# Performance work log

Hardware: AMD Instinct MI355X
Metric: run time of the kernel (lower is better)

## Reference

```python
import jax, jax.numpy as jnp
import numpy as np

NUM_FEATURES = 2048
NUM_SAMPLES = 16384
SOURCE_CLASSES = 1024
TEMP = 0.05
MOMENTUM = 0.2
BATCH = 256
SPECIAL_LABEL = 5554  # hard-coded remap in the original forward (is_source=True path)


def setup_inputs() -> dict:
    key = jax.random.key(0)
    k1, k2, k3 = jax.random.split(key, 3)
    inputs = jax.random.normal(k1, (BATCH, NUM_FEATURES), dtype=jnp.float32)
    inputs = inputs / jnp.linalg.norm(inputs, axis=1, keepdims=True)  # re-ID features are L2-normalized
    targets = jax.random.randint(k2, (BATCH,), 0, NUM_SAMPLES)  # 1-based labels; 0 -> invalid after -1 shift
    features = jax.random.normal(k3, (NUM_SAMPLES, NUM_FEATURES), dtype=jnp.float32)
    features = features / jnp.linalg.norm(features, axis=1, keepdims=True)
    return {"inputs": inputs, "targets": targets, "features": features}


def reference(inputs, targets, features):
    ignore = SOURCE_CLASSES - 1
    t = targets - 1
    t = jnp.where(t == SPECIAL_LABEL, ignore, t)  # remap special label to ignore_index class
    # torch drops rows with t < 0 before the mm and cross_entropy ignores ignore_index;
    # rows are independent under row-wise softmax, so masking is equivalent to filtering.
    valid = (t >= 0) & (t != ignore)
    logits = (inputs @ features.T) / TEMP  # [B, NUM_SAMPLES]
    logp = jax.nn.log_softmax(logits, axis=-1)
    tc = jnp.clip(t, 0, NUM_SAMPLES - 1)
    nll = -jnp.take_along_axis(logp, tc[:, None], axis=1)[:, 0]  # [B]
    n_valid = jnp.sum(valid)
    loss = jnp.sum(jnp.where(valid, nll, 0.0)) / jnp.maximum(n_valid, 1).astype(nll.dtype)
    return loss
```

## Files before the change

### kernel.cpp

```cpp
#include <hip/hip_runtime.h>
#include <hip/hip_bf16.h>

typedef __attribute__((ext_vector_type(4))) float f32x4;
typedef __attribute__((ext_vector_type(8))) short s16x8;

#define M_DIM 256
#define N_DIM 16384
#define K_DIM 2048
#define BM 128
#define BN 128
#define BK 32
#define LDS_PITCH 40
#define NKT (K_DIM / BK)
#define TEMP_INV 20.0f
#define SPECIAL 5554
#define IGNORE_IDX 1023

__device__ __forceinline__ short f2bf(float x) {
  __hip_bfloat16 h = __float2bfloat16(x);
  return __builtin_bit_cast(short, h);
}

__device__ __forceinline__ void cvt_store(short* dst, const float4& f0, const float4& f1) {
  s16x8 h;
  h[0] = f2bf(f0.x); h[1] = f2bf(f0.y); h[2] = f2bf(f0.z); h[3] = f2bf(f0.w);
  h[4] = f2bf(f1.x); h[5] = f2bf(f1.y); h[6] = f2bf(f1.z); h[7] = f2bf(f1.w);
  *reinterpret_cast<s16x8*>(dst) = h;
}

__global__ __launch_bounds__(512, 1) void gemm_logits(
    const float* __restrict__ A, const float* __restrict__ B,
    float* __restrict__ C) {
  __shared__ __align__(16) short As[2][BM * LDS_PITCH];
  __shared__ __align__(16) short Bs[2][BN * LDS_PITCH];

  int bid = blockIdx.x;
  int lbid = (bid & 7) * 32 + (bid >> 3);
  int bm = lbid & 1;
  int bn = lbid >> 1;

  int tid = threadIdx.x;
  int wave = tid >> 6;
  int lane = tid & 63;
  int wm = wave >> 2;
  int wn = wave & 3;

  int srow = tid >> 2;
  int squad = tid & 3;
  const float* aG = A + (size_t)(bm * BM + srow) * K_DIM + squad * 8;
  const float* bG = B + (size_t)(bn * BN + srow) * K_DIM + squad * 8;
  int swoff = srow * LDS_PITCH + squad * 8;

  f32x4 acc[4][2];
#pragma unroll
  for (int mi = 0; mi < 4; ++mi)
#pragma unroll
    for (int ni = 0; ni < 2; ++ni)
      acc[mi][ni] = f32x4{0.f, 0.f, 0.f, 0.f};

  float4 rA[2][2], rB[2][2];

  rA[0][0] = *(const float4*)(aG);      rA[0][1] = *(const float4*)(aG + 4);
  rB[0][0] = *(const float4*)(bG);      rB[0][1] = *(const float4*)(bG + 4);
  cvt_store(&As[0][swoff], rA[0][0], rA[0][1]);
  cvt_store(&Bs[0][swoff], rB[0][0], rB[0][1]);
  rA[1][0] = *(const float4*)(aG + BK); rA[1][1] = *(const float4*)(aG + BK + 4);
  rB[1][0] = *(const float4*)(bG + BK); rB[1][1] = *(const float4*)(bG + BK + 4);
  __syncthreads();

  int arow0 = (wm * 64 + (lane & 15)) * LDS_PITCH + (lane >> 4) * 8;
  int brow0 = (wn * 32 + (lane & 15)) * LDS_PITCH + (lane >> 4) * 8;

  for (int ktb = 0; ktb < NKT; ktb += 2) {
#pragma unroll
    for (int u = 0; u < 2; ++u) {
      int kt = ktb + u;
      const short* asb = &As[u][0];
      const short* bsb = &Bs[u][0];
      s16x8 af[4], bfr[2];
#pragma unroll
      for (int mi = 0; mi < 4; ++mi)
        af[mi] = *reinterpret_cast<const s16x8*>(asb + arow0 + mi * 16 * LDS_PITCH);
#pragma unroll
      for (int ni = 0; ni < 2; ++ni)
        bfr[ni] = *reinterpret_cast<const s16x8*>(bsb + brow0 + ni * 16 * LDS_PITCH);
#pragma unroll
      for (int mi = 0; mi < 4; ++mi)
#pragma unroll
        for (int ni = 0; ni < 2; ++ni)
          acc[mi][ni] = __builtin_amdgcn_mfma_f32_16x16x32_bf16(
              af[mi], bfr[ni], acc[mi][ni], 0, 0, 0);

      if (kt + 1 < NKT) {
        cvt_store(&As[u ^ 1][swoff], rA[u ^ 1][0], rA[u ^ 1][1]);
        cvt_store(&Bs[u ^ 1][swoff], rB[u ^ 1][0], rB[u ^ 1][1]);
        if (kt + 2 < NKT) {
          const float* ap = aG + (size_t)(kt + 2) * BK;
          const float* bp = bG + (size_t)(kt + 2) * BK;
          rA[u][0] = *(const float4*)ap;  rA[u][1] = *(const float4*)(ap + 4);
          rB[u][0] = *(const float4*)bp;  rB[u][1] = *(const float4*)(bp + 4);
        }
        __syncthreads();
      }
    }
  }

  int gm_base = bm * BM + wm * 64 + ((lane >> 4) << 2);
  int gn_base = bn * BN + wn * 32 + (lane & 15);
#pragma unroll
  for (int mi = 0; mi < 4; ++mi)
#pragma unroll
    for (int ni = 0; ni < 2; ++ni)
#pragma unroll
      for (int r = 0; r < 4; ++r)
        C[(size_t)(gm_base + mi * 16 + r) * N_DIM + gn_base + ni * 16] =
            acc[mi][ni][r] * TEMP_INV;
}

__global__ __launch_bounds__(256) void lse_nll(
    const float* __restrict__ logits, const int* __restrict__ targets,
    float* __restrict__ nll, float* __restrict__ vld) {
  int b = blockIdx.x;
  const float* row = logits + (size_t)b * N_DIM;
  const float4* r4 = reinterpret_cast<const float4*>(row);
  __shared__ float sm[8];
  int tid = threadIdx.x;
  int wid = tid >> 6, lane = tid & 63;

  float mx = -1e30f;
  for (int j = tid; j < N_DIM / 4; j += 256) {
    float4 v = r4[j];
    mx = fmaxf(mx, fmaxf(fmaxf(v.x, v.y), fmaxf(v.z, v.w)));
  }
#pragma unroll
  for (int m = 1; m < 64; m <<= 1) mx = fmaxf(mx, __shfl_xor(mx, m, 64));
  if (lane == 0) sm[wid] = mx;
  __syncthreads();
  if (tid == 0) {
    float m2 = fmaxf(fmaxf(sm[0], sm[1]), fmaxf(sm[2], sm[3]));
    sm[0] = m2;
  }
  __syncthreads();
  mx = sm[0];

  float s = 0.f;
  for (int j = tid; j < N_DIM / 4; j += 256) {
    float4 v = r4[j];
    s += __expf(v.x - mx) + __expf(v.y - mx) + __expf(v.z - mx) + __expf(v.w - mx);
  }
#pragma unroll
  for (int m = 1; m < 64; m <<= 1) s += __shfl_xor(s, m, 64);
  __syncthreads();
  if (lane == 0) sm[wid] = s;
  __syncthreads();
  if (tid == 0) {
    float ss = sm[0] + sm[1] + sm[2] + sm[3];
    int t = targets[b] - 1;
    if (t == SPECIAL) t = IGNORE_IDX;
    bool valid = (t >= 0) && (t != IGNORE_IDX);
    int tc = t < 0 ? 0 : (t > N_DIM - 1 ? N_DIM - 1 : t);
    float lse = mx + __logf(ss);
    float nl = lse - row[tc];
    nll[b] = valid ? nl : 0.0f;
    vld[b] = valid ? 1.0f : 0.0f;
  }
}

__global__ __launch_bounds__(256) void final_reduce(
    const float* __restrict__ nll, const float* __restrict__ vld,
    float* __restrict__ out) {
  int tid = threadIdx.x;
  float s = nll[tid];
  float c = vld[tid];
#pragma unroll
  for (int m = 1; m < 64; m <<= 1) {
    s += __shfl_xor(s, m, 64);
    c += __shfl_xor(c, m, 64);
  }
  __shared__ float ss[4], cc[4];
  int wid = tid >> 6, lane = tid & 63;
  if (lane == 0) { ss[wid] = s; cc[wid] = c; }
  __syncthreads();
  if (tid == 0) {
    float S = ss[0] + ss[1] + ss[2] + ss[3];
    float C = cc[0] + cc[1] + cc[2] + cc[3];
    out[0] = S / fmaxf(C, 1.0f);
  }
}

extern "C" void kernel_launch(void* const* d_in, const int* in_sizes, int n_in,
                              void* d_out, int out_size, void* d_ws, size_t ws_size,
                              hipStream_t stream) {
  const float* inputs   = (const float*)d_in[0];
  const int*   targets  = (const int*)d_in[1];
  const float* features = (const float*)d_in[2];
  float* out = (float*)d_out;

  float* logits = (float*)d_ws;
  float* nll    = logits + (size_t)M_DIM * N_DIM;
  float* vld    = nll + M_DIM;

  gemm_logits<<<dim3(256), dim3(512), 0, stream>>>(inputs, features, logits);
  lse_nll<<<dim3(M_DIM), dim3(256), 0, stream>>>(logits, targets, nll, vld);
  final_reduce<<<dim3(1), dim3(256), 0, stream>>>(nll, vld, out);
}
```

Baseline: 47.35 us.

## Fuse log-sum-exp into GEMM epilogue and drop logits materialization

The GEMM epilogue now computes exp of each scaled logit, reduces per-row partial sums across lanes and waves, and writes one partial per row per column tile. It also captures the target logit directly, so the 16 MB logits matrix is never written or reread and the separate lse kernel is removed. The max subtraction is dropped because normalized inputs and temperature 0.05 bound logits to about ±20, which fits in float exp. That relies on the inputs being L2-normalized, and the finalize kernel now sums 128 partials per row serially.

```diff
diff --git a/kernel.cpp b/kernel.cpp
--- a/kernel.cpp
+++ b/kernel.cpp
@@ -28,11 +28,15 @@
   *reinterpret_cast<s16x8*>(dst) = h;
 }
 
-__global__ __launch_bounds__(512, 1) void gemm_logits(
+__global__ __launch_bounds__(512, 1) void gemm_fused(
     const float* __restrict__ A, const float* __restrict__ B,
-    float* __restrict__ C) {
+    const int* __restrict__ targets,
+    float* __restrict__ partial,
+    float* __restrict__ targ) {
   __shared__ __align__(16) short As[2][BM * LDS_PITCH];
   __shared__ __align__(16) short Bs[2][BN * LDS_PITCH];
+  __shared__ int tcs[BM];
+  __shared__ float rsum[BM][4];
 
   int bid = blockIdx.x;
   int lbid = (bid & 7) * 32 + (bid >> 3);
@@ -44,6 +48,13 @@
   int lane = tid & 63;
   int wm = wave >> 2;
   int wn = wave & 3;
+
+  if (tid < BM) {
+    int tt = targets[bm * BM + tid] - 1;
+    if (tt == SPECIAL) tt = IGNORE_IDX;
+    int tc = tt < 0 ? 0 : (tt > N_DIM - 1 ? N_DIM - 1 : tt);
+    tcs[tid] = tc;
+  }
 
   int srow = tid >> 2;
   int squad = tid & 3;
@@ -105,83 +116,56 @@
     }
   }
 
-  int gm_base = bm * BM + wm * 64 + ((lane >> 4) << 2);
-  int gn_base = bn * BN + wn * 32 + (lane & 15);
+  int g = lane >> 4;
+  int cl = lane & 15;
+  int gcol_base = bn * BN + wn * 32 + cl;
 #pragma unroll
-  for (int mi = 0; mi < 4; ++mi)
+  for (int mi = 0; mi < 4; ++mi) {
 #pragma unroll
-    for (int ni = 0; ni < 2; ++ni)
+    for (int r = 0; r < 4; ++r) {
+      int rl = wm * 64 + mi * 16 + g * 4 + r;
+      int tc = tcs[rl];
+      float s = 0.f;
 #pragma unroll
-      for (int r = 0; r < 4; ++r)
-        C[(size_t)(gm_base + mi * 16 + r) * N_DIM + gn_base + ni * 16] =
-            acc[mi][ni][r] * TEMP_INV;
-}
-
-__global__ __launch_bounds__(256) void lse_nll(
-    const float* __restrict__ logits, const int* __restrict__ targets,
-    float* __restrict__ nll, float* __restrict__ vld) {
-  int b = blockIdx.x;
-  const float* row = logits + (size_t)b * N_DIM;
-  const float4* r4 = reinterpret_cast<const float4*>(row);
-  __shared__ float sm[8];
-  int tid = threadIdx.x;
-  int wid = tid >> 6, lane = tid & 63;
-
-  float mx = -1e30f;
-  for (int j = tid; j < N_DIM / 4; j += 256) {
-    float4 v = r4[j];
-    mx = fmaxf(mx, fmaxf(fmaxf(v.x, v.y), fmaxf(v.z, v.w)));
-  }
+      for (int ni = 0; ni < 2; ++ni) {
+        float logit = acc[mi][ni][r] * TEMP_INV;
+        if (gcol_base + ni * 16 == tc) targ[bm * BM + rl] = logit;
+        s += __expf(logit);
+      }
 #pragma unroll
-  for (int m = 1; m < 64; m <<= 1) mx = fmaxf(mx, __shfl_xor(mx, m, 64));
-  if (lane == 0) sm[wid] = mx;
-  __syncthreads();
-  if (tid == 0) {
-    float m2 = fmaxf(fmaxf(sm[0], sm[1]), fmaxf(sm[2], sm[3]));
-    sm[0] = m2;
+      for (int m = 1; m < 16; m <<= 1) s += __shfl_xor(s, m, 64);
+      if (cl == 0) rsum[rl][wn] = s;
+    }
   }
   __syncthreads();
-  mx = sm[0];
-
-  float s = 0.f;
-  for (int j = tid; j < N_DIM / 4; j += 256) {
-    float4 v = r4[j];
-    s += __expf(v.x - mx) + __expf(v.y - mx) + __expf(v.z - mx) + __expf(v.w - mx);
-  }
-#pragma unroll
-  for (int m = 1; m < 64; m <<= 1) s += __shfl_xor(s, m, 64);
-  __syncthreads();
-  if (lane == 0) sm[wid] = s;
-  __syncthreads();
-  if (tid == 0) {
-    float ss = sm[0] + sm[1] + sm[2] + sm[3];
-    int t = targets[b] - 1;
-    if (t == SPECIAL) t = IGNORE_IDX;
-    bool valid = (t >= 0) && (t != IGNORE_IDX);
-    int tc = t < 0 ? 0 : (t > N_DIM - 1 ? N_DIM - 1 : t);
-    float lse = mx + __logf(ss);
-    float nl = lse - row[tc];
-    nll[b] = valid ? nl : 0.0f;
-    vld[b] = valid ? 1.0f : 0.0f;
+  if (tid < BM) {
+    float s = rsum[tid][0] + rsum[tid][1] + rsum[tid][2] + rsum[tid][3];
+    partial[(size_t)bn * M_DIM + bm * BM + tid] = s;
   }
 }
 
-__global__ __launch_bounds__(256) void final_reduce(
-    const float* __restrict__ nll, const float* __restrict__ vld,
-    float* __restrict__ out) {
-  int tid = threadIdx.x;
-  float s = nll[tid];
-  float c = vld[tid];
+__global__ __launch_bounds__(256) void finalize(
+    const float* __restrict__ partial, const float* __restrict__ targ,
+    const int* __restrict__ targets, float* __restrict__ out) {
+  int r = threadIdx.x;
+  float s = 0.f;
+  for (int j = 0; j < 128; ++j) s += partial[(size_t)j * M_DIM + r];
+  int t = targets[r] - 1;
+  if (t == SPECIAL) t = IGNORE_IDX;
+  bool valid = (t >= 0) && (t != IGNORE_IDX);
+  float nl = logf(s) - targ[r];
+  float sv = valid ? nl : 0.0f;
+  float cv = valid ? 1.0f : 0.0f;
 #pragma unroll
   for (int m = 1; m < 64; m <<= 1) {
-    s += __shfl_xor(s, m, 64);
-    c += __shfl_xor(c, m, 64);
+    sv += __shfl_xor(sv, m, 64);
+    cv += __shfl_xor(cv, m, 64);
   }
   __shared__ float ss[4], cc[4];
-  int wid = tid >> 6, lane = tid & 63;
-  if (lane == 0) { ss[wid] = s; cc[wid] = c; }
+  int wid = r >> 6, lane = r & 63;
+  if (lane == 0) { ss[wid] = sv; cc[wid] = cv; }
   __syncthreads();
-  if (tid == 0) {
+  if (r == 0) {
     float S = ss[0] + ss[1] + ss[2] + ss[3];
     float C = cc[0] + cc[1] + cc[2] + cc[3];
     out[0] = S / fmaxf(C, 1.0f);
@@ -196,11 +180,9 @@
   const float* features = (const float*)d_in[2];
   float* out = (float*)d_out;
 
-  float* logits = (float*)d_ws;
-  float* nll    = logits + (size_t)M_DIM * N_DIM;
-  float* vld    = nll + M_DIM;
+  float* partial = (float*)d_ws;
+  float* targ    = partial + (size_t)128 * M_DIM;
 
-  gemm_logits<<<dim3(256), dim3(512), 0, stream>>>(inputs, features, logits);
-  lse_nll<<<dim3(M_DIM), dim3(256), 0, stream>>>(logits, targets, nll, vld);
-  final_reduce<<<dim3(1), dim3(256), 0, stream>>>(nll, vld, out);
+  gemm_fused<<<dim3(256), dim3(512), 0, stream>>>(inputs, features, targets, partial, targ);
+  finalize<<<dim3(1), dim3(256), 0, stream>>>(partial, targ, targets, out);
 }
```

New measurement: 43.04 us. 9.1% less time.
